# Kernel tuning notes

Measured on AMD Instinct MI355X. Metric: run time of the kernel, lower is better.

The kernel has to match this reference:

```python
import jax, jax.numpy as jnp
import numpy as np

N_NODES = 50000
N_EDGES = 800000
IN_C, HID_C, OUT_C = 128, 128, 64
BN_EPS = 1e-5


def setup_inputs() -> dict:
    key = jax.random.key(0)
    ks = jax.random.split(key, 12)
    def lin(k, fan_in, fan_out):
        bound = 1.0 / np.sqrt(fan_in)
        kw, kb = jax.random.split(k)
        W = jax.random.uniform(kw, (fan_in, fan_out), jnp.float32, -bound, bound)
        b = jax.random.uniform(kb, (fan_out,), jnp.float32, -bound, bound)
        return W, b
    x = jax.random.normal(ks[0], (N_NODES, IN_C), jnp.float32)
    edge_index = jax.random.randint(ks[1], (2, N_EDGES), 0, N_NODES, jnp.int32)
    w1a, b1a = lin(ks[2], IN_C, HID_C)
    w1b, b1b = lin(ks[3], HID_C, HID_C)
    w2a, b2a = lin(ks[4], HID_C, OUT_C)
    w2b, b2b = lin(ks[5], OUT_C, OUT_C)
    return {
        "x": x, "edge_index": edge_index,
        "w1a": w1a, "b1a": b1a, "g1": jnp.ones((HID_C,)), "be1": jnp.zeros((HID_C,)),
        "w1b": w1b, "b1b": b1b,
        "w2a": w2a, "b2a": b2a, "g2": jnp.ones((OUT_C,)), "be2": jnp.zeros((OUT_C,)),
        "w2b": w2b, "b2b": b2b,
    }


def _batchnorm(h, gamma, beta):
    # training-style BN over node dim, biased variance (torch BatchNorm1d)
    mean = jnp.mean(h, axis=0)
    var = jnp.mean(jnp.square(h - mean), axis=0)
    return (h - mean) * jax.lax.rsqrt(var + BN_EPS) * gamma + beta


def _gin_layer(x, src, dst, n_nodes, w_a, b_a, gamma, beta, w_b, b_b):
    # GINConv with eps=0: MLP(x + sum_{j->i} x_j)
    agg = jax.ops.segment_sum(x[src], dst, num_segments=n_nodes)  # [N, C]
    h = x + agg
    h = h @ w_a + b_a
    h = jax.nn.relu(_batchnorm(h, gamma, beta))
    return h @ w_b + b_b


def reference(x, edge_index, w1a, b1a, g1, be1, w1b, b1b, w2a, b2a, g2, be2, w2b, b2b):
    src, dst = edge_index[0], edge_index[1]
    n = x.shape[0]
    h = _gin_layer(x, src, dst, n, w1a, b1a, g1, be1, w1b, b1b)
    h = jax.nn.relu(h)  # dropout p=0.0 -> identity
    h = _gin_layer(h, src, dst, n, w2a, b2a, g2, be2, w2b, b2b)
    return jax.nn.log_softmax(h, axis=-1)
```

## Files before the change

### kernel.cpp

```cpp
#include <hip/hip_runtime.h>


typedef unsigned short u16;
typedef unsigned int u32;
typedef __attribute__((ext_vector_type(8))) short short8;
typedef __attribute__((ext_vector_type(4))) short short4v;
typedef __attribute__((ext_vector_type(4))) float f32x4;

#define DEV_INLINE __device__ __forceinline__

DEV_INLINE void atomAddF(float* p, float v) { unsafeAtomicAdd(p, v); }

DEV_INLINE u16 f2bf(float f) {
    unsigned u = __float_as_uint(f);
    u += 0x7fffu + ((u >> 16) & 1u);
    return (u16)(u >> 16);
}
DEV_INLINE float bf2f(u16 h) { return __uint_as_float(((unsigned)h) << 16); }

__global__ __launch_bounds__(256) void wprep4_k(
    const float* __restrict__ w1a, const float* __restrict__ w1b,
    const float* __restrict__ w2a, const float* __restrict__ w2b,
    short* __restrict__ o1a, short* __restrict__ o1b,
    short* __restrict__ o2a, short* __restrict__ o2b)
{
    int b = blockIdx.x;
    const float* W; short* wf; int K, NOUT;
    if (b < 8)       { W = w1a; wf = o1a; K = 128; NOUT = 128; }
    else if (b < 16) { W = w1b; wf = o1b; K = 128; NOUT = 128; b -= 8; }
    else if (b < 20) { W = w2a; wf = o2a; K = 128; NOUT = 64;  b -= 16; }
    else             { W = w2b; wf = o2b; K = 64;  NOUT = 64;  b -= 20; }
    const int u = b * 256 + threadIdx.x;
    const int units = (NOUT / 16) * (K / 32) * 64;
    if (u >= units) return;
    const int per_ct = (K / 32) * 64;
    const int ct = u / per_ct;
    const int rem = u % per_ct;
    const int kc = rem >> 6;
    const int l = rem & 63;
    const int col = ct * 16 + (l & 15);
    const int k0 = kc * 32 + (l >> 4) * 8;
    short8 pk;
#pragma unroll
    for (int j = 0; j < 8; j++)
        pk[j] = (short)f2bf(W[(size_t)(k0 + j) * NOUT + col]);
    *(short8*)&wf[(size_t)u * 8] = pk;
}

template <int KD, int NC, bool ABF16, bool BNIN, bool BIAS, bool RELUOUT,
          bool LOGSM, bool OBF16>
__global__ __launch_bounds__(256) void mgemm(
    const void* __restrict__ Ap, const short* __restrict__ Wf,
    const float* __restrict__ sc, const float* __restrict__ sh,
    const float* __restrict__ bias, void* __restrict__ outp, int M)
{
    constexpr int BM = 128;
    constexpr int KC = KD / 32;
    constexpr int CT = NC / 16;
    __shared__ short Asl[BM * KD];
    __shared__ short Bsl[NC * KD];

    const int t = threadIdx.x;
    const int l = t & 63;
    const int w = t >> 6;

    {
        const float4* src = (const float4*)Wf;
        float4* dst = (float4*)Bsl;
        constexpr int NU = NC * KD / 8;
#pragma unroll
        for (int u = t; u < NU; u += 256) dst[u] = src[u];
    }
    {
        const int r = t >> 1;
        const int half = t & 1;
        const int grow = blockIdx.x * BM + r;
        const int rt = r >> 4;
        constexpr int KH = KD / 2;
        u16 hv[KH];
        if (grow < M) {
            if constexpr (ABF16) {
                const u16* ap = (const u16*)Ap + (size_t)grow * KD + half * KH;
#pragma unroll
                for (int i = 0; i < KH / 8; i++)
                    *(short8*)&hv[i * 8] = ((const short8*)ap)[i];
                if constexpr (BNIN) {
#pragma unroll
                    for (int i = 0; i < KH; i++) {
                        const int k = half * KH + i;
                        hv[i] = f2bf(fmaxf(0.f, bf2f(hv[i]) * sc[k] + sh[k]));
                    }
                }
            } else {
                const float* ap = (const float*)Ap + (size_t)grow * KD + half * KH;
#pragma unroll
                for (int i = 0; i < KH / 4; i++) {
                    const float4 v = ((const float4*)ap)[i];
                    float f0 = v.x, f1 = v.y, f2 = v.z, f3 = v.w;
                    if constexpr (BNIN) {
                        const int k = half * KH + i * 4;
                        f0 = fmaxf(0.f, f0 * sc[k + 0] + sh[k + 0]);
                        f1 = fmaxf(0.f, f1 * sc[k + 1] + sh[k + 1]);
                        f2 = fmaxf(0.f, f2 * sc[k + 2] + sh[k + 2]);
                        f3 = fmaxf(0.f, f3 * sc[k + 3] + sh[k + 3]);
                    }
                    hv[i * 4 + 0] = f2bf(f0); hv[i * 4 + 1] = f2bf(f1);
                    hv[i * 4 + 2] = f2bf(f2); hv[i * 4 + 3] = f2bf(f3);
                }
            }
        } else {
#pragma unroll
            for (int i = 0; i < KH; i++) hv[i] = 0;
        }
#pragma unroll
        for (int g = 0; g < KH / 8; g++) {
            const int k0 = half * KH + g * 8;
            const int kc = k0 >> 5;
            const int lane = (r & 15) + ((k0 >> 3) & 3) * 16;
            *(short8*)&Asl[((rt * KC + kc) * 64 + lane) * 8] =
                *(short8*)&hv[g * 8];
        }
    }
    __syncthreads();

    const int rt0 = w * 2;
    f32x4 acc[2][CT];
#pragma unroll
    for (int i = 0; i < 2; i++)
#pragma unroll
        for (int c = 0; c < CT; c++) acc[i][c] = (f32x4){0.f, 0.f, 0.f, 0.f};

#pragma unroll
    for (int kc = 0; kc < KC; kc++) {
        const short8 x0 = *(const short8*)&Asl[((rt0 * KC + kc) * 64 + l) * 8];
        const short8 x1 = *(const short8*)&Asl[(((rt0 + 1) * KC + kc) * 64 + l) * 8];
#pragma unroll
        for (int ct = 0; ct < CT; ct++) {
            const short8 wb = *(const short8*)&Bsl[((ct * KC + kc) * 64 + l) * 8];
            acc[0][ct] = __builtin_amdgcn_mfma_f32_16x16x32_bf16(wb, x0, acc[0][ct], 0, 0, 0);
            acc[1][ct] = __builtin_amdgcn_mfma_f32_16x16x32_bf16(wb, x1, acc[1][ct], 0, 0, 0);
        }
    }

    const int cbase = (l >> 4) * 4;
#pragma unroll
    for (int rr = 0; rr < 2; rr++) {
        const int grow = blockIdx.x * BM + (rt0 + rr) * 16 + (l & 15);
        if constexpr (!LOGSM) {
            if (grow < M) {
#pragma unroll
                for (int ct = 0; ct < CT; ct++) {
                    f32x4 o = acc[rr][ct];
                    if constexpr (BIAS) {
                        const float4 bv = *(const float4*)&bias[ct * 16 + cbase];
                        o[0] += bv.x; o[1] += bv.y; o[2] += bv.z; o[3] += bv.w;
                    }
                    if constexpr (RELUOUT) {
#pragma unroll
                        for (int j = 0; j < 4; j++) o[j] = fmaxf(o[j], 0.f);
                    }
                    if constexpr (OBF16) {
                        short4v o16;
#pragma unroll
                        for (int j = 0; j < 4; j++) o16[j] = (short)f2bf(o[j]);
                        *(short4v*)&((u16*)outp)[(size_t)grow * NC + ct * 16 + cbase] = o16;
                    } else {
                        *(f32x4*)&((float*)outp)[(size_t)grow * NC + ct * 16 + cbase] = o;
                    }
                }
            }
        } else {
            float v[CT * 4];
#pragma unroll
            for (int ct = 0; ct < CT; ct++) {
                const float4 bv = *(const float4*)&bias[ct * 16 + cbase];
                v[ct * 4 + 0] = acc[rr][ct][0] + bv.x;
                v[ct * 4 + 1] = acc[rr][ct][1] + bv.y;
                v[ct * 4 + 2] = acc[rr][ct][2] + bv.z;
                v[ct * 4 + 3] = acc[rr][ct][3] + bv.w;
            }
            float m = v[0];
#pragma unroll
            for (int j = 1; j < CT * 4; j++) m = fmaxf(m, v[j]);
            m = fmaxf(m, __shfl_xor(m, 16));
            m = fmaxf(m, __shfl_xor(m, 32));
            float s = 0.f;
#pragma unroll
            for (int j = 0; j < CT * 4; j++) s += __expf(v[j] - m);
            s += __shfl_xor(s, 16);
            s += __shfl_xor(s, 32);
            const float lg = m + __logf(s);
            if (grow < M) {
#pragma unroll
                for (int ct = 0; ct < CT; ct++) {
                    f32x4 o;
#pragma unroll
                    for (int j = 0; j < 4; j++) o[j] = v[ct * 4 + j] - lg;
                    *(f32x4*)&((float*)outp)[(size_t)grow * NC + ct * 16 + cbase] = o;
                }
            }
        }
    }
}

__global__ __launch_bounds__(256) void hist_k(const int* __restrict__ ei,
                                              int* __restrict__ cnt, int E)
{
    const int gid = blockIdx.x * blockDim.x + threadIdx.x;
    const int stride = gridDim.x * blockDim.x;
    for (int e = gid; e < E; e += stride) atomicAdd(&cnt[ei[E + e]], 1);
}

__global__ __launch_bounds__(256) void bsum_k(const int* __restrict__ cnt,
                                              int* __restrict__ bsum, int N)
{
    __shared__ int ws[4];
    const int i = blockIdx.x * 256 + threadIdx.x;
    int v = (i < N) ? cnt[i] : 0;
    for (int d = 32; d; d >>= 1) v += __shfl_xor(v, d, 64);
    if ((threadIdx.x & 63) == 0) ws[threadIdx.x >> 6] = v;
    __syncthreads();
    if (threadIdx.x == 0) bsum[blockIdx.x] = ws[0] + ws[1] + ws[2] + ws[3];
}

__global__ __launch_bounds__(256) void bscan_k(const int* __restrict__ bsum,
                                               int* __restrict__ bpre, int G1)
{
    __shared__ int part[256];
    const int t = threadIdx.x;
    const int v = (t < G1) ? bsum[t] : 0;
    part[t] = v;
    __syncthreads();
    for (int d = 1; d < 256; d <<= 1) {
        const int u = (t >= d) ? part[t - d] : 0;
        __syncthreads();
        part[t] += u;
        __syncthreads();
    }
    bpre[t] = part[t] - v;
}

__global__ __launch_bounds__(256) void offs_k(const int* __restrict__ cnt,
                                              const int* __restrict__ bpre,
                                              int* __restrict__ off,
                                              int* __restrict__ cursor,
                                              int N, int E)
{
    __shared__ int part[256];
    const int t = threadIdx.x;
    const int i = blockIdx.x * 256 + t;
    const int v = (i < N) ? cnt[i] : 0;
    part[t] = v;
    __syncthreads();
    for (int d = 1; d < 256; d <<= 1) {
        const int u = (t >= d) ? part[t - d] : 0;
        __syncthreads();
        part[t] += u;
        __syncthreads();
    }
    if (i < N) {
        const int o = bpre[blockIdx.x] + part[t] - v;
        off[i] = o;
        cursor[i] = o;
    }
    if (blockIdx.x == 0 && t == 0) off[N] = E;
}

__global__ __launch_bounds__(256) void fill_k(const int* __restrict__ ei,
                                              int* __restrict__ cursor,
                                              int* __restrict__ srcs, int E)
{
    const int gid = blockIdx.x * blockDim.x + threadIdx.x;
    const int stride = gridDim.x * blockDim.x;
    for (int e = gid; e < E; e += stride) {
        const int s = ei[e];
        const int d = ei[E + e];
        const int pos = atomicAdd(&cursor[d], 1);
        srcs[pos] = s;
    }
}

template <int C>
__global__ __launch_bounds__(256) void segsum_bf(
    const u16* __restrict__ p, const int* __restrict__ off,
    const int* __restrict__ srcs, u16* __restrict__ out,
    float* __restrict__ sum, float* __restrict__ sumsq, int N)
{
    constexpr int BLKN = 8;
    constexpr int VPL = C / 64;
    __shared__ float red[4][64][2 * VPL];

    const int wv = threadIdx.x >> 6;
    const int l  = threadIdx.x & 63;
    const int base = blockIdx.x * 4 * BLKN;

    float ss[VPL], qq[VPL];
#pragma unroll
    for (int v = 0; v < VPL; v++) { ss[v] = 0.f; qq[v] = 0.f; }

    for (int i = 0; i < BLKN; i++) {
        const int n = base + i * 4 + wv;
        if (n < N) {
            const int lo = __builtin_amdgcn_readfirstlane(off[n]);
            const int hi = __builtin_amdgcn_readfirstlane(off[n + 1]);
            float acc[VPL];
            if constexpr (VPL == 2) {
                const u32 u = *(const u32*)&p[(size_t)n * C + 2 * l];
                acc[0] = bf2f((u16)u);
                acc[1] = bf2f((u16)(u >> 16));
            } else {
                acc[0] = bf2f(p[(size_t)n * C + l]);
            }
            const int cnt = hi - lo;
            if (cnt > 0) {
                const int last = hi - 1;
                int idx[8];
#pragma unroll
                for (int j = 0; j < 8; j++) idx[j] = srcs[min(lo + j, last)];
                for (int e = lo; e < hi; e += 8) {
                    int nx[8];
#pragma unroll
                    for (int j = 0; j < 8; j++)
                        nx[j] = srcs[min(e + 8 + j, last)];
#pragma unroll
                    for (int j = 0; j < 8; j++) {
                        const bool live = (e + j) < hi;
                        if constexpr (VPL == 2) {
                            const u32 u = *(const u32*)&p[(size_t)idx[j] * C + 2 * l];
                            const float v0 = bf2f((u16)u);
                            const float v1 = bf2f((u16)(u >> 16));
                            acc[0] += live ? v0 : 0.f;
                            acc[1] += live ? v1 : 0.f;
                        } else {
                            const float v = bf2f(p[(size_t)idx[j] * C + l]);
                            acc[0] += live ? v : 0.f;
                        }
                    }
#pragma unroll
                    for (int j = 0; j < 8; j++) idx[j] = nx[j];
                }
            }
            if constexpr (VPL == 2) {
                const u16 r0 = f2bf(acc[0]);
                const u16 r1 = f2bf(acc[1]);
                *(u32*)&out[(size_t)n * C + 2 * l] = (u32)r0 | ((u32)r1 << 16);
                const float f0 = bf2f(r0), f1 = bf2f(r1);
                ss[0] += f0; qq[0] += f0 * f0;
                ss[1] += f1; qq[1] += f1 * f1;
            } else {
                const u16 r = f2bf(acc[0]);
                out[(size_t)n * C + l] = r;
                const float f = bf2f(r);
                ss[0] += f; qq[0] += f * f;
            }
        }
    }

#pragma unroll
    for (int v = 0; v < VPL; v++) {
        red[wv][l][2 * v] = ss[v];
        red[wv][l][2 * v + 1] = qq[v];
    }
    __syncthreads();
    if (wv == 0) {
#pragma unroll
        for (int v = 0; v < VPL; v++) {
            float a = 0.f, b = 0.f;
#pragma unroll
            for (int w2 = 0; w2 < 4; w2++) {
                a += red[w2][l][2 * v];
                b += red[w2][l][2 * v + 1];
            }
            const int ch = (VPL == 2) ? (2 * l + v) : l;
            atomAddF(&sum[ch], a);
            atomAddF(&sumsq[ch], b);
        }
    }
}

__global__ void bnfinal_k(const float* __restrict__ sum,
                          const float* __restrict__ sumsq,
                          const float* __restrict__ g,
                          const float* __restrict__ be,
                          float* __restrict__ sc, float* __restrict__ sh,
                          int C, float invN)
{
    const int c = threadIdx.x;
    if (c < C) {
        const float m = sum[c] * invN;
        const float v = sumsq[c] * invN - m * m;
        const float r = rsqrtf(v + 1e-5f);
        const float s = g[c] * r;
        sc[c] = s;
        sh[c] = be[c] - m * s;
    }
}

extern "C" void kernel_launch(void* const* d_in, const int* in_sizes, int n_in,
                              void* d_out, int out_size, void* d_ws, size_t ws_size,
                              hipStream_t stream)
{
    const float* x   = (const float*)d_in[0];
    const int*   ei  = (const int*)d_in[1];
    const float* w1a = (const float*)d_in[2];
    const float* g1  = (const float*)d_in[4];
    const float* be1 = (const float*)d_in[5];
    const float* w1b = (const float*)d_in[6];
    const float* b1b = (const float*)d_in[7];
    const float* w2a = (const float*)d_in[8];
    const float* g2  = (const float*)d_in[10];
    const float* be2 = (const float*)d_in[11];
    const float* w2b = (const float*)d_in[12];
    const float* b2b = (const float*)d_in[13];
    float* out = (float*)d_out;

    const int N = in_sizes[0] / 128;
    const int E = in_sizes[1] / 2;

    u16* buf1 = (u16*)d_ws;
    u16* buf2 = buf1 + (size_t)N * 128;
    float* stats = (float*)(buf2 + (size_t)N * 128);
    float* sum1 = stats,       *sq1 = stats + 128;
    float* sum2 = stats + 256, *sq2 = stats + 320;
    float* sc1  = stats + 384, *sh1 = stats + 512;
    float* sc2  = stats + 640, *sh2 = stats + 704;
    int* cnt    = (int*)(stats + 1024);
    int* off    = cnt + N;
    int* cursor = off + N + 1;
    int* srcs   = cursor + N;
    int* bsum   = srcs + E;
    int* bpre   = bsum + 256;
    short* w1af = (short*)(bpre + 256);
    short* w1bf = w1af + 128 * 128;
    short* w2af = w1bf + 128 * 128;
    short* w2bf = w2af + 128 * 64;
    u16* p1 = buf1;
    u16* s1 = buf2;
    u16* h1 = buf1;
    u16* p2 = buf2;
    u16* s2 = buf2 + (size_t)N * 64;

    hipMemsetAsync(stats, 0, 1024 * sizeof(float) + (size_t)N * sizeof(int), stream);

    const int G1 = (N + 255) / 256;
    const int gb = (N + 127) / 128;
    const int gs = (N + 31) / 32;

    hist_k<<<1024, 256, 0, stream>>>(ei, cnt, E);
    bsum_k<<<G1, 256, 0, stream>>>(cnt, bsum, N);
    bscan_k<<<1, 256, 0, stream>>>(bsum, bpre, G1);
    offs_k<<<G1, 256, 0, stream>>>(cnt, bpre, off, cursor, N, E);
    fill_k<<<1024, 256, 0, stream>>>(ei, cursor, srcs, E);

    wprep4_k<<<22, 256, 0, stream>>>(w1a, w1b, w2a, w2b, w1af, w1bf, w2af, w2bf);

    mgemm<128, 128, false, false, false, false, false, true>
        <<<gb, 256, 0, stream>>>(x, w1af, nullptr, nullptr, nullptr, p1, N);
    segsum_bf<128><<<gs, 256, 0, stream>>>(p1, off, srcs, s1, sum1, sq1, N);
    bnfinal_k<<<1, 128, 0, stream>>>(sum1, sq1, g1, be1, sc1, sh1, 128, 1.f / N);
    mgemm<128, 128, true, true, true, true, false, true>
        <<<gb, 256, 0, stream>>>(s1, w1bf, sc1, sh1, b1b, h1, N);

    mgemm<128, 64, true, false, false, false, false, true>
        <<<gb, 256, 0, stream>>>(h1, w2af, nullptr, nullptr, nullptr, p2, N);
    segsum_bf<64><<<gs, 256, 0, stream>>>(p2, off, srcs, s2, sum2, sq2, N);
    bnfinal_k<<<1, 64, 0, stream>>>(sum2, sq2, g2, be2, sc2, sh2, 64, 1.f / N);
    mgemm<64, 64, true, true, true, false, true, false>
        <<<gb, 256, 0, stream>>>(s2, w2bf, sc2, sh2, b2b, out, N);
}
```

Before: 309.1 us.

## Load edge indices wave-wide once and broadcast via readlane in segsum

The CSR gather-sum kernel now loads up to 64 source indices in one coalesced wave-wide load and broadcasts each to all lanes with readlane. This replaces the per-lane redundant scalar index loads and the prefetch double-buffer. It also halves the nodes per block and doubles the grid, with a launch-bounds occupancy hint, to expose more parallelism. The cost is extra readlane instructions and more blocks doing the stats reduction and atomics.

```diff
diff --git a/kernel.cpp b/kernel.cpp
--- a/kernel.cpp
+++ b/kernel.cpp
@@ -280,13 +280,35 @@
     }
 }
 
+template <int C, int VPL>
+DEV_INLINE void gath8(const u16* __restrict__ p, int iv, int g, int l, int m,
+                      float acc[VPL])
+{
+    u32 u[8];
+#pragma unroll
+    for (int j = 0; j < 8; j++) {
+        const int s = __builtin_amdgcn_readlane(iv, g * 8 + j);
+        if constexpr (VPL == 2)
+            u[j] = *(const u32*)&p[(size_t)s * C + 2 * l];
+        else
+            u[j] = p[(size_t)s * C + l];
+    }
+#pragma unroll
+    for (int j = 0; j < 8; j++) {
+        if (j < m) {
+            acc[0] += bf2f((u16)u[j]);
+            if constexpr (VPL == 2) acc[1] += bf2f((u16)(u[j] >> 16));
+        }
+    }
+}
+
 template <int C>
-__global__ __launch_bounds__(256) void segsum_bf(
+__global__ __launch_bounds__(256, 4) void segsum_bf(
     const u16* __restrict__ p, const int* __restrict__ off,
     const int* __restrict__ srcs, u16* __restrict__ out,
     float* __restrict__ sum, float* __restrict__ sumsq, int N)
 {
-    constexpr int BLKN = 8;
+    constexpr int BLKN = 4;
     constexpr int VPL = C / 64;
     __shared__ float red[4][64][2 * VPL];
 
@@ -311,33 +333,20 @@
             } else {
                 acc[0] = bf2f(p[(size_t)n * C + l]);
             }
-            const int cnt = hi - lo;
-            if (cnt > 0) {
-                const int last = hi - 1;
-                int idx[8];
-#pragma unroll
-                for (int j = 0; j < 8; j++) idx[j] = srcs[min(lo + j, last)];
-                for (int e = lo; e < hi; e += 8) {
-                    int nx[8];
-#pragma unroll
-                    for (int j = 0; j < 8; j++)
-                        nx[j] = srcs[min(e + 8 + j, last)];
-#pragma unroll
-                    for (int j = 0; j < 8; j++) {
-                        const bool live = (e + j) < hi;
-                        if constexpr (VPL == 2) {
-                            const u32 u = *(const u32*)&p[(size_t)idx[j] * C + 2 * l];
-                            const float v0 = bf2f((u16)u);
-                            const float v1 = bf2f((u16)(u >> 16));
-                            acc[0] += live ? v0 : 0.f;
-                            acc[1] += live ? v1 : 0.f;
-                        } else {
-                            const float v = bf2f(p[(size_t)idx[j] * C + l]);
-                            acc[0] += live ? v : 0.f;
-                        }
-                    }
-#pragma unroll
-                    for (int j = 0; j < 8; j++) idx[j] = nx[j];
+            int e = lo;
+            for (; e + 64 <= hi; e += 64) {
+                const int iv = srcs[e + l];
+#pragma unroll
+                for (int g = 0; g < 8; g++)
+                    gath8<C, VPL>(p, iv, g, l, 8, acc);
+            }
+            if (e < hi) {
+                const int rem = hi - e;
+                const int iv = srcs[min(e + l, hi - 1)];
+#pragma unroll
+                for (int g = 0; g < 8; g++) {
+                    if (g * 8 < rem)
+                        gath8<C, VPL>(p, iv, g, l, min(rem - g * 8, 8), acc);
                 }
             }
             if constexpr (VPL == 2) {
@@ -444,7 +453,7 @@
 
     const int G1 = (N + 255) / 256;
     const int gb = (N + 127) / 128;
-    const int gs = (N + 31) / 32;
+    const int gs = (N + 15) / 16;
 
     hist_k<<<1024, 256, 0, stream>>>(ei, cnt, E);
     bsum_k<<<G1, 256, 0, stream>>>(cnt, bsum, N);
```

Result: slower. 413.9 us (+33.9%).

## Pack src/dst edges into u32 and aggregate per node-block with LDS atomics

Applied to the files above, without the earlier changes.

The CSR fill now stores each edge as a 32-bit word holding a 16-bit source and a 16-bit destination. Segment-sum becomes edge-parallel: each block stages the edge list of a 32-node range in LDS, waves gather source rows in groups of four edges, and they accumulate into a shared float tile with LDS atomics. The aim is to balance work across waves regardless of node degree, replacing the one-wave-per-node serial loop. In exchange it adds LDS atomic traffic, keeps only four gathers in flight with narrower 16-bit loads, and assumes node ids fit in 16 bits.

```diff
diff --git a/kernel.cpp b/kernel.cpp
--- a/kernel.cpp
+++ b/kernel.cpp
@@ -268,7 +268,7 @@
 
 __global__ __launch_bounds__(256) void fill_k(const int* __restrict__ ei,
                                               int* __restrict__ cursor,
-                                              int* __restrict__ srcs, int E)
+                                              u32* __restrict__ epack, int E)
 {
     const int gid = blockIdx.x * blockDim.x + threadIdx.x;
     const int stride = gridDim.x * blockDim.x;
@@ -276,90 +276,92 @@
         const int s = ei[e];
         const int d = ei[E + e];
         const int pos = atomicAdd(&cursor[d], 1);
-        srcs[pos] = s;
+        epack[pos] = (u32)s | ((u32)d << 16);
     }
 }
 
 template <int C>
-__global__ __launch_bounds__(256) void segsum_bf(
+__global__ __launch_bounds__(256) void segsum_ep(
     const u16* __restrict__ p, const int* __restrict__ off,
-    const int* __restrict__ srcs, u16* __restrict__ out,
+    const u32* __restrict__ epack, u16* __restrict__ out,
     float* __restrict__ sum, float* __restrict__ sumsq, int N)
 {
-    constexpr int BLKN = 8;
+    constexpr int NB = 32;
     constexpr int VPL = C / 64;
-    __shared__ float red[4][64][2 * VPL];
-
-    const int wv = threadIdx.x >> 6;
-    const int l  = threadIdx.x & 63;
-    const int base = blockIdx.x * 4 * BLKN;
+    constexpr int EBUF = 1024;
+    __shared__ float acc[NB][C];
+    __shared__ u32 ebuf[EBUF];
+
+    const int tid = threadIdx.x;
+    const int wv = tid >> 6;
+    const int l = tid & 63;
+    const int n0 = blockIdx.x * NB;
+    const int nend = min(n0 + NB, N);
+    const int elo = off[n0];
+    const int ehi = off[nend];
+
+    for (int i = tid; i < NB * C; i += 256) (&acc[0][0])[i] = 0.f;
+
+    for (int ebase = elo; ebase < ehi; ebase += EBUF) {
+        const int ecnt = min(EBUF, ehi - ebase);
+        __syncthreads();
+        for (int k = tid; k < ecnt; k += 256) ebuf[k] = epack[ebase + k];
+        __syncthreads();
+
+        const int ngrp = (ecnt + 3) / 4;
+        for (int g = wv; g < ngrp; g += 4) {
+            const int e0 = g * 4;
+            const int m = min(4, ecnt - e0);
+            u32 pk[4];
+#pragma unroll
+            for (int j = 0; j < 4; j++) pk[j] = ebuf[e0 + (j < m ? j : 0)];
+            u16 ga[4], gb[4];
+#pragma unroll
+            for (int j = 0; j < 4; j++) {
+                const int s = (int)(pk[j] & 0xFFFFu);
+                ga[j] = p[(size_t)s * C + l];
+                if constexpr (VPL == 2) gb[j] = p[(size_t)s * C + 64 + l];
+            }
+#pragma unroll
+            for (int j = 0; j < 4; j++) {
+                if (j < m) {
+                    const int d = (int)(pk[j] >> 16) - n0;
+                    atomicAdd(&acc[d][l], bf2f(ga[j]));
+                    if constexpr (VPL == 2)
+                        atomicAdd(&acc[d][64 + l], bf2f(gb[j]));
+                }
+            }
+        }
+    }
+    __syncthreads();
 
     float ss[VPL], qq[VPL];
 #pragma unroll
     for (int v = 0; v < VPL; v++) { ss[v] = 0.f; qq[v] = 0.f; }
 
-    for (int i = 0; i < BLKN; i++) {
-        const int n = base + i * 4 + wv;
-        if (n < N) {
-            const int lo = __builtin_amdgcn_readfirstlane(off[n]);
-            const int hi = __builtin_amdgcn_readfirstlane(off[n + 1]);
-            float acc[VPL];
-            if constexpr (VPL == 2) {
-                const u32 u = *(const u32*)&p[(size_t)n * C + 2 * l];
-                acc[0] = bf2f((u16)u);
-                acc[1] = bf2f((u16)(u >> 16));
-            } else {
-                acc[0] = bf2f(p[(size_t)n * C + l]);
-            }
-            const int cnt = hi - lo;
-            if (cnt > 0) {
-                const int last = hi - 1;
-                int idx[8];
-#pragma unroll
-                for (int j = 0; j < 8; j++) idx[j] = srcs[min(lo + j, last)];
-                for (int e = lo; e < hi; e += 8) {
-                    int nx[8];
-#pragma unroll
-                    for (int j = 0; j < 8; j++)
-                        nx[j] = srcs[min(e + 8 + j, last)];
-#pragma unroll
-                    for (int j = 0; j < 8; j++) {
-                        const bool live = (e + j) < hi;
-                        if constexpr (VPL == 2) {
-                            const u32 u = *(const u32*)&p[(size_t)idx[j] * C + 2 * l];
-                            const float v0 = bf2f((u16)u);
-                            const float v1 = bf2f((u16)(u >> 16));
-                            acc[0] += live ? v0 : 0.f;
-                            acc[1] += live ? v1 : 0.f;
-                        } else {
-                            const float v = bf2f(p[(size_t)idx[j] * C + l]);
-                            acc[0] += live ? v : 0.f;
-                        }
-                    }
-#pragma unroll
-                    for (int j = 0; j < 8; j++) idx[j] = nx[j];
-                }
-            }
-            if constexpr (VPL == 2) {
-                const u16 r0 = f2bf(acc[0]);
-                const u16 r1 = f2bf(acc[1]);
-                *(u32*)&out[(size_t)n * C + 2 * l] = (u32)r0 | ((u32)r1 << 16);
-                const float f0 = bf2f(r0), f1 = bf2f(r1);
-                ss[0] += f0; qq[0] += f0 * f0;
-                ss[1] += f1; qq[1] += f1 * f1;
-            } else {
-                const u16 r = f2bf(acc[0]);
-                out[(size_t)n * C + l] = r;
+    for (int i = 0; i < NB / 4; i++) {
+        const int n = i * 4 + wv;
+        const int gn = n0 + n;
+        if (gn < N) {
+#pragma unroll
+            for (int v = 0; v < VPL; v++) {
+                const int ch = v * 64 + l;
+                const float val = acc[n][ch] + bf2f(p[(size_t)gn * C + ch]);
+                const u16 r = f2bf(val);
+                out[(size_t)gn * C + ch] = r;
                 const float f = bf2f(r);
-                ss[0] += f; qq[0] += f * f;
-            }
-        }
-    }
-
+                ss[v] += f;
+                qq[v] += f * f;
+            }
+        }
+    }
+
+    float* red = (float*)ebuf;
+    __syncthreads();
 #pragma unroll
     for (int v = 0; v < VPL; v++) {
-        red[wv][l][2 * v] = ss[v];
-        red[wv][l][2 * v + 1] = qq[v];
+        red[v * 512 + tid] = ss[v];
+        red[v * 512 + 256 + tid] = qq[v];
     }
     __syncthreads();
     if (wv == 0) {
@@ -368,12 +370,11 @@
             float a = 0.f, b = 0.f;
 #pragma unroll
             for (int w2 = 0; w2 < 4; w2++) {
-                a += red[w2][l][2 * v];
-                b += red[w2][l][2 * v + 1];
-            }
-            const int ch = (VPL == 2) ? (2 * l + v) : l;
-            atomAddF(&sum[ch], a);
-            atomAddF(&sumsq[ch], b);
+                a += red[v * 512 + w2 * 64 + l];
+                b += red[v * 512 + 256 + w2 * 64 + l];
+            }
+            atomAddF(&sum[v * 64 + l], a);
+            atomAddF(&sumsq[v * 64 + l], b);
         }
     }
 }
@@ -427,8 +428,8 @@
     int* cnt    = (int*)(stats + 1024);
     int* off    = cnt + N;
     int* cursor = off + N + 1;
-    int* srcs   = cursor + N;
-    int* bsum   = srcs + E;
+    u32* epack  = (u32*)(cursor + N);
+    int* bsum   = (int*)(epack + E);
     int* bpre   = bsum + 256;
     short* w1af = (short*)(bpre + 256);
     short* w1bf = w1af + 128 * 128;
@@ -450,20 +451,20 @@
     bsum_k<<<G1, 256, 0, stream>>>(cnt, bsum, N);
     bscan_k<<<1, 256, 0, stream>>>(bsum, bpre, G1);
     offs_k<<<G1, 256, 0, stream>>>(cnt, bpre, off, cursor, N, E);
-    fill_k<<<1024, 256, 0, stream>>>(ei, cursor, srcs, E);
+    fill_k<<<1024, 256, 0, stream>>>(ei, cursor, epack, E);
 
     wprep4_k<<<22, 256, 0, stream>>>(w1a, w1b, w2a, w2b, w1af, w1bf, w2af, w2bf);
 
     mgemm<128, 128, false, false, false, false, false, true>
         <<<gb, 256, 0, stream>>>(x, w1af, nullptr, nullptr, nullptr, p1, N);
-    segsum_bf<128><<<gs, 256, 0, stream>>>(p1, off, srcs, s1, sum1, sq1, N);
+    segsum_ep<128><<<gs, 256, 0, stream>>>(p1, off, epack, s1, sum1, sq1, N);
     bnfinal_k<<<1, 128, 0, stream>>>(sum1, sq1, g1, be1, sc1, sh1, 128, 1.f / N);
     mgemm<128, 128, true, true, true, true, false, true>
         <<<gb, 256, 0, stream>>>(s1, w1bf, sc1, sh1, b1b, h1, N);
 
     mgemm<128, 64, true, false, false, false, false, true>
         <<<gb, 256, 0, stream>>>(h1, w2af, nullptr, nullptr, nullptr, p2, N);
-    segsum_bf<64><<<gs, 256, 0, stream>>>(p2, off, srcs, s2, sum2, sq2, N);
+    segsum_ep<64><<<gs, 256, 0, stream>>>(p2, off, epack, s2, sum2, sq2, N);
     bnfinal_k<<<1, 64, 0, stream>>>(sum2, sq2, g2, be2, sc2, sh2, 64, 1.f / N);
     mgemm<64, 64, true, true, true, false, true, false>
         <<<gb, 256, 0, stream>>>(s2, w2bf, sc2, sh2, b2b, out, N);
```

After: 1.073 ms. 3.47x slower.

## Split segment-sum gather into 32-channel slices per block

Applied to the files above, without the earlier changes.

Replaces the segment-sum kernel with a sliced variant. Each block now covers one 32-channel slice of a 32-node chunk, so each gathered row read is 64 bytes. Block indices interleave the slices of the same chunk, and a per-slice reduction feeds the BatchNorm statistics atomics. In exchange, the whole wave repeats the same loads across 64 lanes while only 16 lanes store, and the edge-index traversal is repeated once per slice, which adds loop and index-load work.

```diff
diff --git a/kernel.cpp b/kernel.cpp
--- a/kernel.cpp
+++ b/kernel.cpp
@@ -281,100 +281,90 @@
 }
 
 template <int C>
-__global__ __launch_bounds__(256) void segsum_bf(
+__global__ __launch_bounds__(256) void segsum_sl(
     const u16* __restrict__ p, const int* __restrict__ off,
     const int* __restrict__ srcs, u16* __restrict__ out,
     float* __restrict__ sum, float* __restrict__ sumsq, int N)
 {
     constexpr int BLKN = 8;
-    constexpr int VPL = C / 64;
-    __shared__ float red[4][64][2 * VPL];
+    __shared__ float red[4][16][4];
 
     const int wv = threadIdx.x >> 6;
     const int l  = threadIdx.x & 63;
-    const int base = blockIdx.x * 4 * BLKN;
-
-    float ss[VPL], qq[VPL];
-#pragma unroll
-    for (int v = 0; v < VPL; v++) { ss[v] = 0.f; qq[v] = 0.f; }
-
-    for (int i = 0; i < BLKN; i++) {
-        const int n = base + i * 4 + wv;
-        if (n < N) {
-            const int lo = __builtin_amdgcn_readfirstlane(off[n]);
-            const int hi = __builtin_amdgcn_readfirstlane(off[n + 1]);
-            float acc[VPL];
-            if constexpr (VPL == 2) {
-                const u32 u = *(const u32*)&p[(size_t)n * C + 2 * l];
-                acc[0] = bf2f((u16)u);
-                acc[1] = bf2f((u16)(u >> 16));
-            } else {
-                acc[0] = bf2f(p[(size_t)n * C + l]);
-            }
-            const int cnt = hi - lo;
-            if (cnt > 0) {
-                const int last = hi - 1;
-                int idx[8];
-#pragma unroll
-                for (int j = 0; j < 8; j++) idx[j] = srcs[min(lo + j, last)];
-                for (int e = lo; e < hi; e += 8) {
-                    int nx[8];
-#pragma unroll
-                    for (int j = 0; j < 8; j++)
-                        nx[j] = srcs[min(e + 8 + j, last)];
-#pragma unroll
-                    for (int j = 0; j < 8; j++) {
-                        const bool live = (e + j) < hi;
-                        if constexpr (VPL == 2) {
-                            const u32 u = *(const u32*)&p[(size_t)idx[j] * C + 2 * l];
+    const int sub = l & 15;
+
+    const int nchunks = (N + 31) / 32;
+    const int x = blockIdx.x & 7;
+    const int g = blockIdx.x >> 3;
+    int slice, chunk;
+    if constexpr (C == 128) { slice = x & 3; chunk = g * 2 + (x >> 2); }
+    else                    { slice = x & 1; chunk = g * 4 + (x >> 1); }
+    const int soff = slice * 32;
+
+    float ss0 = 0.f, ss1 = 0.f, qq0 = 0.f, qq1 = 0.f;
+
+    if (chunk < nchunks) {
+        const int base = chunk * 32;
+        for (int i = 0; i < BLKN; i++) {
+            const int n = base + i * 4 + wv;
+            if (n < N) {
+                const int lo = __builtin_amdgcn_readfirstlane(off[n]);
+                const int hi = __builtin_amdgcn_readfirstlane(off[n + 1]);
+                const u32 u0 = *(const u32*)&p[(size_t)n * C + soff + sub * 2];
+                float acc0 = bf2f((u16)u0);
+                float acc1 = bf2f((u16)(u0 >> 16));
+                if (lo < hi) {
+                    const int last = hi - 1;
+                    int idx[8];
+#pragma unroll
+                    for (int j = 0; j < 8; j++) idx[j] = srcs[min(lo + j, last)];
+                    for (int e = lo; e < hi; e += 8) {
+                        int nx[8];
+#pragma unroll
+                        for (int j = 0; j < 8; j++)
+                            nx[j] = srcs[min(e + 8 + j, last)];
+#pragma unroll
+                        for (int j = 0; j < 8; j++) {
+                            const bool live = (e + j) < hi;
+                            const u32 u = *(const u32*)&p[(size_t)idx[j] * C + soff + sub * 2];
                             const float v0 = bf2f((u16)u);
                             const float v1 = bf2f((u16)(u >> 16));
-                            acc[0] += live ? v0 : 0.f;
-                            acc[1] += live ? v1 : 0.f;
-                        } else {
-                            const float v = bf2f(p[(size_t)idx[j] * C + l]);
-                            acc[0] += live ? v : 0.f;
+                            acc0 += live ? v0 : 0.f;
+                            acc1 += live ? v1 : 0.f;
                         }
-                    }
-#pragma unroll
-                    for (int j = 0; j < 8; j++) idx[j] = nx[j];
+#pragma unroll
+                        for (int j = 0; j < 8; j++) idx[j] = nx[j];
+                    }
                 }
+                const u16 r0 = f2bf(acc0);
+                const u16 r1 = f2bf(acc1);
+                if (l < 16)
+                    *(u32*)&out[(size_t)n * C + soff + sub * 2] =
+                        (u32)r0 | ((u32)r1 << 16);
+                const float f0 = bf2f(r0), f1 = bf2f(r1);
+                ss0 += f0; qq0 += f0 * f0;
+                ss1 += f1; qq1 += f1 * f1;
             }
-            if constexpr (VPL == 2) {
-                const u16 r0 = f2bf(acc[0]);
-                const u16 r1 = f2bf(acc[1]);
-                *(u32*)&out[(size_t)n * C + 2 * l] = (u32)r0 | ((u32)r1 << 16);
-                const float f0 = bf2f(r0), f1 = bf2f(r1);
-                ss[0] += f0; qq[0] += f0 * f0;
-                ss[1] += f1; qq[1] += f1 * f1;
-            } else {
-                const u16 r = f2bf(acc[0]);
-                out[(size_t)n * C + l] = r;
-                const float f = bf2f(r);
-                ss[0] += f; qq[0] += f * f;
-            }
-        }
-    }
-
-#pragma unroll
-    for (int v = 0; v < VPL; v++) {
-        red[wv][l][2 * v] = ss[v];
-        red[wv][l][2 * v + 1] = qq[v];
+        }
+    }
+
+    if (l < 16) {
+        red[wv][sub][0] = ss0; red[wv][sub][1] = ss1;
+        red[wv][sub][2] = qq0; red[wv][sub][3] = qq1;
     }
     __syncthreads();
-    if (wv == 0) {
-#pragma unroll
-        for (int v = 0; v < VPL; v++) {
-            float a = 0.f, b = 0.f;
-#pragma unroll
-            for (int w2 = 0; w2 < 4; w2++) {
-                a += red[w2][l][2 * v];
-                b += red[w2][l][2 * v + 1];
-            }
-            const int ch = (VPL == 2) ? (2 * l + v) : l;
-            atomAddF(&sum[ch], a);
-            atomAddF(&sumsq[ch], b);
-        }
+    if (wv == 0 && l < 16 && chunk < nchunks) {
+        float a0 = 0.f, a1 = 0.f, b0 = 0.f, b1 = 0.f;
+#pragma unroll
+        for (int w2 = 0; w2 < 4; w2++) {
+            a0 += red[w2][sub][0]; a1 += red[w2][sub][1];
+            b0 += red[w2][sub][2]; b1 += red[w2][sub][3];
+        }
+        const int ch = soff + sub * 2;
+        atomAddF(&sum[ch], a0);
+        atomAddF(&sum[ch + 1], a1);
+        atomAddF(&sumsq[ch], b0);
+        atomAddF(&sumsq[ch + 1], b1);
     }
 }
 
@@ -444,7 +434,9 @@
 
     const int G1 = (N + 255) / 256;
     const int gb = (N + 127) / 128;
-    const int gs = (N + 31) / 32;
+    const int nchunks = (N + 31) / 32;
+    const int gs1 = 8 * ((nchunks + 1) / 2);
+    const int gs2 = 8 * ((nchunks + 3) / 4);
 
     hist_k<<<1024, 256, 0, stream>>>(ei, cnt, E);
     bsum_k<<<G1, 256, 0, stream>>>(cnt, bsum, N);
@@ -456,14 +448,14 @@
 
     mgemm<128, 128, false, false, false, false, false, true>
         <<<gb, 256, 0, stream>>>(x, w1af, nullptr, nullptr, nullptr, p1, N);
-    segsum_bf<128><<<gs, 256, 0, stream>>>(p1, off, srcs, s1, sum1, sq1, N);
+    segsum_sl<128><<<gs1, 256, 0, stream>>>(p1, off, srcs, s1, sum1, sq1, N);
     bnfinal_k<<<1, 128, 0, stream>>>(sum1, sq1, g1, be1, sc1, sh1, 128, 1.f / N);
     mgemm<128, 128, true, true, true, true, false, true>
         <<<gb, 256, 0, stream>>>(s1, w1bf, sc1, sh1, b1b, h1, N);
 
     mgemm<128, 64, true, false, false, false, false, true>
         <<<gb, 256, 0, stream>>>(h1, w2af, nullptr, nullptr, nullptr, p2, N);
-    segsum_bf<64><<<gs, 256, 0, stream>>>(p2, off, srcs, s2, sum2, sq2, N);
+    segsum_sl<64><<<gs2, 256, 0, stream>>>(p2, off, srcs, s2, sum2, sq2, N);
     bnfinal_k<<<1, 64, 0, stream>>>(sum2, sq2, g2, be2, sc2, sh2, 64, 1.f / N);
     mgemm<64, 64, true, true, true, false, true, false>
         <<<gb, 256, 0, stream>>>(s2, w2bf, sc2, sh2, b2b, out, N);
```

Measured after the change: 375.8 us. 21.6% more time.
